# Kernel optimization log

Hardware: AMD Instinct MI355X
Metric: run time of the kernel (lower is better)

## Reference

```python
import jax, jax.numpy as jnp
import numpy as np

N, D = 2048, 64
H, W = 128, 128
NEAR, RADIUS_CLIP, BLUR = 0.01, 3.0, 0.3
A_MIN, A_MAX = 1.0 / 255.0, 0.999


def setup_inputs():
    key = jax.random.key(0)
    k = jax.random.split(key, 6)
    xy = jax.random.uniform(k[0], (N, 2), minval=-1.2, maxval=1.2)
    zz = jax.random.uniform(k[1], (N, 1), minval=3.0, maxval=5.0)
    means = jnp.concatenate([xy, zz], axis=1).astype(jnp.float32)
    quats = jax.random.normal(k[2], (N, 4), dtype=jnp.float32)
    scales = jax.random.normal(k[3], (N, 3), dtype=jnp.float32) * 0.3 - 2.2  # log-scales
    opacities = jax.random.normal(k[4], (N,), dtype=jnp.float32) * 0.5 + 1.0  # logits
    gs_features = jax.random.normal(k[5], (N, D), dtype=jnp.float32) * 0.5
    c2o = jnp.eye(4, dtype=jnp.float32)
    K = jnp.array([[200.0, 0.0, 64.0], [0.0, 200.0, 64.0], [0.0, 0.0, 1.0]], dtype=jnp.float32)
    return dict(means=means, quats=quats, scales=scales, opacities=opacities,
                gs_features=gs_features, c2o=c2o, K=K, width=W, height=H)


def _quat_to_rot(q):
    q = q / jnp.linalg.norm(q, axis=-1, keepdims=True)
    w, x, y, z = q[:, 0], q[:, 1], q[:, 2], q[:, 3]
    r0 = jnp.stack([1 - 2 * (y * y + z * z), 2 * (x * y - w * z), 2 * (x * z + w * y)], -1)
    r1 = jnp.stack([2 * (x * y + w * z), 1 - 2 * (x * x + z * z), 2 * (y * z - w * x)], -1)
    r2 = jnp.stack([2 * (x * z - w * y), 2 * (y * z + w * x), 1 - 2 * (x * x + y * y)], -1)
    return jnp.stack([r0, r1, r2], -2)  # [N,3,3]


def _rasterize(means, quats, log_scales, opac_logits, colors, viewmat, K, width, height):
    Rv, tv = viewmat[:3, :3], viewmat[:3, 3]
    fx, fy, cx, cy = K[0, 0], K[1, 1], K[0, 2], K[1, 2]
    mc = means @ Rv.T + tv                      # camera-space means [N,3]
    x, y, z = mc[:, 0], mc[:, 1], mc[:, 2]
    # 3D covariance Sigma = R S S^T R^T, rotated into camera frame
    M = _quat_to_rot(quats) * jnp.exp(log_scales)[:, None, :]
    cov_w = M @ jnp.swapaxes(M, 1, 2)           # [N,3,3]
    cov_c = jnp.einsum('ij,njk,lk->nil', Rv, cov_w, Rv)
    # perspective (EWA) Jacobian [N,2,3]
    rz = 1.0 / z
    zero = jnp.zeros_like(z)
    J = jnp.stack([jnp.stack([fx * rz, zero, -fx * x * rz * rz], -1),
                   jnp.stack([zero, fy * rz, -fy * y * rz * rz], -1)], -2)
    cov2d = jnp.einsum('nij,njk,nlk->nil', J, cov_c, J)
    a = cov2d[:, 0, 0] + BLUR
    b = cov2d[:, 0, 1]
    c = cov2d[:, 1, 1] + BLUR
    det = a * c - b * b
    cA, cB, cC = c / det, -b / det, a / det     # conic = inverse 2D covariance
    mx = fx * x * rz + cx
    my = fy * y * rz + cy
    # cull: behind near plane, degenerate, or projected 3-sigma radius below radius_clip
    lam_max = 0.5 * (a + c) + jnp.sqrt(jnp.maximum(0.25 * (a - c) ** 2 + b * b, 1e-12))
    radius = 3.0 * jnp.sqrt(lam_max)
    valid = (z > NEAR) & (det > 0) & (radius > RADIUS_CLIP)
    opac = jax.nn.sigmoid(opac_logits)
    # global front-to-back depth order (single camera)
    order = jnp.argsort(z)
    mx, my, cA, cB, cC = mx[order], my[order], cA[order], cB[order], cC[order]
    opac, valid, colors = opac[order], valid[order], colors[order]
    # per pixel-gaussian evaluation, [H,W,N]
    px = jnp.arange(width, dtype=means.dtype) + 0.5
    py = jnp.arange(height, dtype=means.dtype) + 0.5
    dx = px[None, :, None] - mx[None, None, :]
    dy = py[:, None, None] - my[None, None, :]
    sigma = 0.5 * (cA * dx * dx + cC * dy * dy) + cB * dx * dy
    alpha = jnp.minimum(opac * jnp.exp(-sigma), A_MAX)
    alpha = jnp.where((sigma >= 0) & valid & (alpha >= A_MIN), alpha, 0.0)
    # front-to-back alpha compositing: exclusive transmittance cumprod
    Tcum = jnp.cumprod(1.0 - alpha, axis=-1)
    T_excl = jnp.concatenate([jnp.ones_like(Tcum[..., :1]), Tcum[..., :-1]], axis=-1)
    out = jnp.einsum('hwn,nd->hwd', alpha * T_excl, colors)
    return out[None]  # [1,H,W,D]


def reference(means, quats, scales, opacities, gs_features, c2o, K, width, height):
    viewmat = jnp.linalg.inv(c2o)
    return _rasterize(means, quats, scales, opacities, gs_features, viewmat, K, width, height)
```

## Files before the change

### kernel.cpp

```cpp
#include <hip/hip_runtime.h>

constexpr int NG  = 2048;
constexpr int DF  = 64;
constexpr int IW  = 128;
constexpr int IH  = 128;
constexpr int SEG = 8;
constexpr int RB  = SEG * 64;
constexpr int CAP = 1024;

#define P_NEAR 0.01f
#define P_BLUR 0.3f
#define P_AMIN (1.0f/255.0f)
#define P_AMAX 0.999f

constexpr int L_T    = 0;
constexpr int L_CNT  = 512;
constexpr int L_SIDX = 528;
constexpr int L_ACC  = L_SIDX + CAP;
constexpr int L_PRM  = L_ACC;
constexpr int L_KEYS = L_PRM + CAP * 8;
constexpr int ACC_STRIDE = 66;
constexpr int L_TOTAL = L_ACC + SEG * 64 * ACC_STRIDE;

__device__ inline void invert4x4(const float* m, float* inv) {
    inv[0]  =  m[5]*m[10]*m[15] - m[5]*m[11]*m[14] - m[9]*m[6]*m[15] + m[9]*m[7]*m[14] + m[13]*m[6]*m[11] - m[13]*m[7]*m[10];
    inv[4]  = -m[4]*m[10]*m[15] + m[4]*m[11]*m[14] + m[8]*m[6]*m[15] - m[8]*m[7]*m[14] - m[12]*m[6]*m[11] + m[12]*m[7]*m[10];
    inv[8]  =  m[4]*m[9]*m[15]  - m[4]*m[11]*m[13] - m[8]*m[5]*m[15] + m[8]*m[7]*m[13] + m[12]*m[5]*m[11] - m[12]*m[7]*m[9];
    inv[12] = -m[4]*m[9]*m[14]  + m[4]*m[10]*m[13] + m[8]*m[5]*m[14] - m[8]*m[6]*m[13] - m[12]*m[5]*m[10] + m[12]*m[6]*m[9];
    inv[1]  = -m[1]*m[10]*m[15] + m[1]*m[11]*m[14] + m[9]*m[2]*m[15] - m[9]*m[3]*m[14] - m[13]*m[2]*m[11] + m[13]*m[3]*m[10];
    inv[5]  =  m[0]*m[10]*m[15] - m[0]*m[11]*m[14] - m[8]*m[2]*m[15] + m[8]*m[3]*m[14] + m[12]*m[2]*m[11] - m[12]*m[3]*m[10];
    inv[9]  = -m[0]*m[9]*m[15]  + m[0]*m[11]*m[13] + m[8]*m[1]*m[15] - m[8]*m[3]*m[13] - m[12]*m[1]*m[11] + m[12]*m[3]*m[9];
    inv[13] =  m[0]*m[9]*m[14]  - m[0]*m[10]*m[13] - m[8]*m[1]*m[14] + m[8]*m[2]*m[13] + m[12]*m[1]*m[10] - m[12]*m[2]*m[9];
    inv[2]  =  m[1]*m[6]*m[15]  - m[1]*m[7]*m[14]  - m[5]*m[2]*m[15] + m[5]*m[3]*m[14] + m[13]*m[2]*m[7]  - m[13]*m[3]*m[6];
    inv[6]  = -m[0]*m[6]*m[15]  + m[0]*m[7]*m[14]  + m[4]*m[2]*m[15] - m[4]*m[3]*m[14] - m[12]*m[2]*m[7]  + m[12]*m[3]*m[6];
    inv[10] =  m[0]*m[5]*m[15]  - m[0]*m[7]*m[13]  - m[4]*m[1]*m[15] + m[4]*m[3]*m[13] + m[12]*m[1]*m[7]  - m[12]*m[3]*m[5];
    inv[14] = -m[0]*m[5]*m[14]  + m[0]*m[6]*m[13]  + m[4]*m[1]*m[14] - m[4]*m[2]*m[13] - m[12]*m[1]*m[6]  + m[12]*m[2]*m[5];
    inv[3]  = -m[1]*m[6]*m[11]  + m[1]*m[7]*m[10]  + m[5]*m[2]*m[11] - m[5]*m[3]*m[10] - m[9]*m[2]*m[7]   + m[9]*m[3]*m[6];
    inv[7]  =  m[0]*m[6]*m[11]  - m[0]*m[7]*m[10]  - m[4]*m[2]*m[11] + m[4]*m[3]*m[10] + m[8]*m[2]*m[7]   - m[8]*m[3]*m[6];
    inv[11] = -m[0]*m[5]*m[11]  + m[0]*m[7]*m[9]   + m[4]*m[1]*m[11] - m[4]*m[3]*m[9]  - m[8]*m[1]*m[7]   + m[8]*m[3]*m[5];
    inv[15] =  m[0]*m[5]*m[10]  - m[0]*m[6]*m[9]   - m[4]*m[1]*m[10] + m[4]*m[2]*m[9]  + m[8]*m[1]*m[6]   - m[8]*m[2]*m[5];
    float det = m[0]*inv[0] + m[1]*inv[4] + m[2]*inv[8] + m[3]*inv[12];
    det = 1.0f / det;
    #pragma unroll
    for (int i = 0; i < 16; ++i) inv[i] *= det;
}

__global__ __launch_bounds__(RB) void fused_render_kernel(
    const float* __restrict__ means,  const float* __restrict__ quats,
    const float* __restrict__ scales, const float* __restrict__ opac_logits,
    const float* __restrict__ colors, const float* __restrict__ c2o,
    const float* __restrict__ Kmat,   float* __restrict__ out)
{
    extern __shared__ float lds[];
    int*                cnt  = (int*)(lds + L_CNT);
    int*                sidx = (int*)(lds + L_SIDX);
    unsigned long long* keys = (unsigned long long*)(lds + L_KEYS);
    float4*             prm4 = (float4*)(lds + L_PRM);

    const int tid  = threadIdx.x;
    const int lane = tid & 63;
    const int seg  = tid >> 6;
    const int tile = blockIdx.x;
    const int tx = (tile & 15) * 8;
    const int ty = (tile >> 4) * 8;
    const float px = tx + (lane & 7) + 0.5f;
    const float py = ty + (lane >> 3) + 0.5f;
    const float cxt = tx + 4.0f, cyt = ty + 4.0f;

    if (tid == 0) *cnt = 0;
    __syncthreads();

    {
        float inv[16];
        {
            float m[16];
            #pragma unroll
            for (int t = 0; t < 16; ++t) m[t] = c2o[t];
            invert4x4(m, inv);
        }
        const float fx = Kmat[0], fy = Kmat[4], cx = Kmat[2], cy = Kmat[5];

        for (int c = 0; c < NG / RB; ++c) {
            const int g = c * RB + tid;
            float mx = means[g*3+0], my = means[g*3+1], mz = means[g*3+2];
            float X = inv[0]*mx + inv[1]*my + inv[2]*mz  + inv[3];
            float Y = inv[4]*mx + inv[5]*my + inv[6]*mz  + inv[7];
            float Z = inv[8]*mx + inv[9]*my + inv[10]*mz + inv[11];

            float qw = quats[g*4+0], qx = quats[g*4+1], qy = quats[g*4+2], qz = quats[g*4+3];
            float qn = rsqrtf(qw*qw + qx*qx + qy*qy + qz*qz);
            qw *= qn; qx *= qn; qy *= qn; qz *= qn;
            float R00 = 1.f - 2.f*(qy*qy + qz*qz), R01 = 2.f*(qx*qy - qw*qz), R02 = 2.f*(qx*qz + qw*qy);
            float R10 = 2.f*(qx*qy + qw*qz), R11 = 1.f - 2.f*(qx*qx + qz*qz), R12 = 2.f*(qy*qz - qw*qx);
            float R20 = 2.f*(qx*qz - qw*qy), R21 = 2.f*(qy*qz + qw*qx), R22 = 1.f - 2.f*(qx*qx + qy*qy);

            float s0 = expf(scales[g*3+0]), s1 = expf(scales[g*3+1]), s2 = expf(scales[g*3+2]);
            float M00 = R00*s0, M01 = R01*s1, M02 = R02*s2;
            float M10 = R10*s0, M11 = R11*s1, M12 = R12*s2;
            float M20 = R20*s0, M21 = R21*s1, M22 = R22*s2;

            float V00 = M00*M00 + M01*M01 + M02*M02;
            float V01 = M00*M10 + M01*M11 + M02*M12;
            float V02 = M00*M20 + M01*M21 + M02*M22;
            float V11 = M10*M10 + M11*M11 + M12*M12;
            float V12 = M10*M20 + M11*M21 + M12*M22;
            float V22 = M20*M20 + M21*M21 + M22*M22;

            float Rv[3][3] = {{inv[0],inv[1],inv[2]},{inv[4],inv[5],inv[6]},{inv[8],inv[9],inv[10]}};
            float Vm[3][3] = {{V00,V01,V02},{V01,V11,V12},{V02,V12,V22}};
            float Tm[3][3], C[3][3];
            #pragma unroll
            for (int r = 0; r < 3; ++r)
                #pragma unroll
                for (int cc = 0; cc < 3; ++cc)
                    Tm[r][cc] = Rv[r][0]*Vm[0][cc] + Rv[r][1]*Vm[1][cc] + Rv[r][2]*Vm[2][cc];
            #pragma unroll
            for (int r = 0; r < 3; ++r)
                #pragma unroll
                for (int cc = 0; cc < 3; ++cc)
                    C[r][cc] = Tm[r][0]*Rv[cc][0] + Tm[r][1]*Rv[cc][1] + Tm[r][2]*Rv[cc][2];

            float rz = 1.0f / Z;
            float j00 = fx*rz, j02 = -fx*X*rz*rz;
            float j11 = fy*rz, j12 = -fy*Y*rz*rz;

            float c00 = j00*j00*C[0][0] + 2.f*j00*j02*C[0][2] + j02*j02*C[2][2];
            float c01 = j00*j11*C[0][1] + j00*j12*C[0][2] + j02*j11*C[1][2] + j02*j12*C[2][2];
            float c11 = j11*j11*C[1][1] + 2.f*j11*j12*C[1][2] + j12*j12*C[2][2];

            float a = c00 + P_BLUR;
            float b = c01;
            float cc_ = c11 + P_BLUR;
            float det = a*cc_ - b*b;

            float pmx = fx*X*rz + cx;
            float pmy = fy*Y*rz + cy;

            float lam = 0.5f*(a + cc_) + sqrtf(fmaxf(0.25f*(a - cc_)*(a - cc_) + b*b, 1e-12f));
            float radius = 3.0f * sqrtf(lam);
            bool valid = (Z > P_NEAR) && (det > 0.0f) && (radius > 3.0f);

            float op = 1.0f / (1.0f + expf(-opac_logits[g]));

            bool sel = false;
            float cA = 0.f, cB = 0.f, cC2 = 0.f;
            if (valid) {
                float rdet = 1.0f / det;
                cA = cc_ * rdet; cB = -b * rdet; cC2 = a * rdet;
                float smax = logf(255.0f * op);
                if (smax > 0.f) {
                    float rx = sqrtf(2.f * a   * smax) * 1.0001f + 1e-3f;
                    float ry = sqrtf(2.f * cc_ * smax) * 1.0001f + 1e-3f;
                    sel = (fabsf(pmx - cxt) <= rx + 3.5f) && (fabsf(pmy - cyt) <= ry + 3.5f);
                }
            }

            unsigned long long m = __ballot(sel);
            int wbase = 0;
            if (lane == 0 && m) wbase = atomicAdd(cnt, (int)__popcll(m));
            wbase = __shfl(wbase, 0);
            if (sel) {
                int pos = wbase + (int)__popcll(m & ((1ull << lane) - 1ull));
                if (pos < CAP) {
                    prm4[pos*2]   = make_float4(pmx, pmy, cA, cB);
                    prm4[pos*2+1] = make_float4(cC2, op, __int_as_float(g), 0.f);
                    keys[pos] = ((unsigned long long)__float_as_uint(Z) << 32) | (unsigned)g;
                }
            }
        }
    }
    __syncthreads();
    int L = *cnt;
    if (L > CAP) L = CAP;

    {
        int padL = (L + 1) & ~1;
        if (tid < padL - L) keys[L + tid] = ~0ull;
        __syncthreads();
        const ulonglong2* k2 = (const ulonglong2*)keys;
        for (int k = tid; k < L; k += RB) {
            unsigned long long kk = keys[k];
            int rank = 0;
            #pragma unroll 2
            for (int c = 0; c < padL / 2; ++c) {
                ulonglong2 q = k2[c];
                rank += (q.x < kk) + (q.y < kk);
            }
            sidx[rank] = k;
        }
    }
    __syncthreads();

    float acc[64];
    #pragma unroll
    for (int f = 0; f < 64; ++f) acc[f] = 0.f;
    float T = 1.0f;

    {
        const int r0 = (seg * L) >> 3;
        const int r1 = ((seg + 1) * L) >> 3;
        const float4* cp4 = (const float4*)colors;
        if (r1 > r0) {
            int k = sidx[r0];
            float4 e0 = prm4[k*2], e1 = prm4[k*2+1];
            for (int r = r0; r < r1; ++r) {
                int kn = (r + 1 < r1) ? sidx[r + 1] : k;
                float4 f0 = prm4[kn*2], f1 = prm4[kn*2+1];

                const float4* crow = cp4 + (size_t)(unsigned)__float_as_int(e1.z) * 16;
                float4 cbuf[16];
                #pragma unroll
                for (int q = 0; q < 16; ++q) cbuf[q] = crow[q];

                float dx = px - e0.x, dy = py - e0.y;
                float sig = 0.5f*(e0.z*dx*dx + e1.x*dy*dy) + e0.w*dx*dy;
                float al = fminf(e1.y * __expf(-sig), P_AMAX);
                al = (sig >= 0.f && al >= P_AMIN) ? al : 0.f;

                if (__ballot(al > 0.f)) {
                    float wv = T * al;
                    #pragma unroll
                    for (int q = 0; q < 16; ++q) {
                        acc[4*q+0] = fmaf(wv, cbuf[q].x, acc[4*q+0]);
                        acc[4*q+1] = fmaf(wv, cbuf[q].y, acc[4*q+1]);
                        acc[4*q+2] = fmaf(wv, cbuf[q].z, acc[4*q+2]);
                        acc[4*q+3] = fmaf(wv, cbuf[q].w, acc[4*q+3]);
                    }
                    T *= (1.f - al);
                    if (!__ballot(T >= 1e-6f)) break;
                }
                e0 = f0; e1 = f1; k = kn;
            }
        }
    }

    __syncthreads();
    {
        float* ab = lds + L_ACC + (size_t)(seg * 64 + lane) * ACC_STRIDE;
        #pragma unroll
        for (int q = 0; q < 32; ++q)
            *(float2*)(ab + 2*q) = make_float2(acc[2*q], acc[2*q+1]);
        lds[L_T + seg*64 + lane] = T;
    }
    __syncthreads();

    {
        int p  = tid >> 3;
        int f0 = (tid & 7) * 8;
        float r[8];
        const float* ab = lds + L_ACC + (size_t)((SEG-1)*64 + p) * ACC_STRIDE + f0;
        #pragma unroll
        for (int j = 0; j < 4; ++j) {
            float2 u = *(const float2*)(ab + 2*j);
            r[2*j] = u.x; r[2*j+1] = u.y;
        }
        #pragma unroll
        for (int s = SEG - 2; s >= 0; --s) {
            float Ts = lds[L_T + s*64 + p];
            const float* as_ = lds + L_ACC + (size_t)(s*64 + p) * ACC_STRIDE + f0;
            #pragma unroll
            for (int j = 0; j < 4; ++j) {
                float2 u = *(const float2*)(as_ + 2*j);
                r[2*j]   = fmaf(Ts, r[2*j],   u.x);
                r[2*j+1] = fmaf(Ts, r[2*j+1], u.y);
            }
        }
        int pyg = ty + (p >> 3), pxg = tx + (p & 7);
        float* op_ = out + (size_t)(pyg * IW + pxg) * DF + f0;
        *(float4*)op_       = make_float4(r[0], r[1], r[2], r[3]);
        *(float4*)(op_ + 4) = make_float4(r[4], r[5], r[6], r[7]);
    }
}

extern "C" void kernel_launch(void* const* d_in, const int* in_sizes, int n_in,
                              void* d_out, int out_size, void* d_ws, size_t ws_size,
                              hipStream_t stream) {
    const float* means  = (const float*)d_in[0];
    const float* quats  = (const float*)d_in[1];
    const float* scales = (const float*)d_in[2];
    const float* opac   = (const float*)d_in[3];
    const float* colors = (const float*)d_in[4];
    const float* c2o    = (const float*)d_in[5];
    const float* Kmat   = (const float*)d_in[6];
    float* out = (float*)d_out;
    (void)d_ws; (void)ws_size;

    (void)hipFuncSetAttribute((const void*)fused_render_kernel,
                              hipFuncAttributeMaxDynamicSharedMemorySize,
                              L_TOTAL * 4);

    fused_render_kernel<<<IH*IW/64, RB, L_TOTAL*4, stream>>>(
        means, quats, scales, opac, colors, c2o, Kmat, out);
}
```

Measured before the change: 118.7 us.

## Split each tile's depth range across 16 waves with a chunked LDS reduction

Each 8x8 tile's sorted Gaussian list is now split into 16 depth segments instead of 8, so the block runs 1024 threads and each wave composites a shorter run of Gaussians. The per-segment accumulator merge is redone in four 16-feature chunks with a narrower LDS stride, so the reduction buffer stays small while sharing space with the parameter area. The sort loop drops to a single pass per thread, since the block now has at least as many threads as list entries. The aim is more latency hiding per CU on the serial compositing loop. In exchange it risks register spills, because the 64-float accumulator must fit a 1024-thread block, and it adds extra barriers and wasted work in later segments that cannot stop early on transmittance.

```diff
diff --git a/kernel.cpp b/kernel.cpp
--- a/kernel.cpp
+++ b/kernel.cpp
@@ -4,7 +4,7 @@
 constexpr int DF  = 64;
 constexpr int IW  = 128;
 constexpr int IH  = 128;
-constexpr int SEG = 8;
+constexpr int SEG = 16;
 constexpr int RB  = SEG * 64;
 constexpr int CAP = 1024;
 
@@ -14,13 +14,14 @@
 #define P_AMAX 0.999f
 
 constexpr int L_T    = 0;
-constexpr int L_CNT  = 512;
-constexpr int L_SIDX = 528;
-constexpr int L_ACC  = L_SIDX + CAP;
-constexpr int L_PRM  = L_ACC;
+constexpr int L_CNT  = 1024;
+constexpr int L_SIDX = 1040;
+constexpr int L_OVL  = L_SIDX + CAP;
+constexpr int L_PRM  = L_OVL;
 constexpr int L_KEYS = L_PRM + CAP * 8;
-constexpr int ACC_STRIDE = 66;
-constexpr int L_TOTAL = L_ACC + SEG * 64 * ACC_STRIDE;
+constexpr int L_ACC  = L_OVL;
+constexpr int ACC_ST = 18;
+constexpr int L_TOTAL = L_OVL + SEG * 64 * ACC_ST;
 
 __device__ inline void invert4x4(const float* m, float* inv) {
     inv[0]  =  m[5]*m[10]*m[15] - m[5]*m[11]*m[14] - m[9]*m[6]*m[15] + m[9]*m[7]*m[14] + m[13]*m[6]*m[11] - m[13]*m[7]*m[10];
@@ -80,6 +81,7 @@
         }
         const float fx = Kmat[0], fy = Kmat[4], cx = Kmat[2], cy = Kmat[5];
 
+        #pragma unroll
         for (int c = 0; c < NG / RB; ++c) {
             const int g = c * RB + tid;
             float mx = means[g*3+0], my = means[g*3+1], mz = means[g*3+2];
@@ -178,15 +180,15 @@
         if (tid < padL - L) keys[L + tid] = ~0ull;
         __syncthreads();
         const ulonglong2* k2 = (const ulonglong2*)keys;
-        for (int k = tid; k < L; k += RB) {
-            unsigned long long kk = keys[k];
+        if (tid < L) {
+            unsigned long long kk = keys[tid];
             int rank = 0;
             #pragma unroll 2
             for (int c = 0; c < padL / 2; ++c) {
                 ulonglong2 q = k2[c];
                 rank += (q.x < kk) + (q.y < kk);
             }
-            sidx[rank] = k;
+            sidx[rank] = tid;
         }
     }
     __syncthreads();
@@ -197,8 +199,8 @@
     float T = 1.0f;
 
     {
-        const int r0 = (seg * L) >> 3;
-        const int r1 = ((seg + 1) * L) >> 3;
+        const int r0 = (seg * L) >> 4;
+        const int r1 = ((seg + 1) * L) >> 4;
         const float4* cp4 = (const float4*)colors;
         if (r1 > r0) {
             int k = sidx[r0];
@@ -234,41 +236,32 @@
         }
     }
 
-    __syncthreads();
-    {
-        float* ab = lds + L_ACC + (size_t)(seg * 64 + lane) * ACC_STRIDE;
+    lds[L_T + seg*64 + lane] = T;
+    __syncthreads();
+
+    const int p_  = tid >> 4;
+    const int f_  = tid & 15;
+    const int pyg = ty + (p_ >> 3), pxg = tx + (p_ & 7);
+    float* opix = out + (size_t)(pyg * IW + pxg) * DF + f_;
+
+    #pragma unroll
+    for (int c = 0; c < 4; ++c) {
+        float* ab = lds + L_ACC + (size_t)(seg * 64 + lane) * ACC_ST;
         #pragma unroll
-        for (int q = 0; q < 32; ++q)
-            *(float2*)(ab + 2*q) = make_float2(acc[2*q], acc[2*q+1]);
-        lds[L_T + seg*64 + lane] = T;
-    }
-    __syncthreads();
-
-    {
-        int p  = tid >> 3;
-        int f0 = (tid & 7) * 8;
-        float r[8];
-        const float* ab = lds + L_ACC + (size_t)((SEG-1)*64 + p) * ACC_STRIDE + f0;
-        #pragma unroll
-        for (int j = 0; j < 4; ++j) {
-            float2 u = *(const float2*)(ab + 2*j);
-            r[2*j] = u.x; r[2*j+1] = u.y;
-        }
-        #pragma unroll
-        for (int s = SEG - 2; s >= 0; --s) {
-            float Ts = lds[L_T + s*64 + p];
-            const float* as_ = lds + L_ACC + (size_t)(s*64 + p) * ACC_STRIDE + f0;
-            #pragma unroll
-            for (int j = 0; j < 4; ++j) {
-                float2 u = *(const float2*)(as_ + 2*j);
-                r[2*j]   = fmaf(Ts, r[2*j],   u.x);
-                r[2*j+1] = fmaf(Ts, r[2*j+1], u.y);
-            }
-        }
-        int pyg = ty + (p >> 3), pxg = tx + (p & 7);
-        float* op_ = out + (size_t)(pyg * IW + pxg) * DF + f0;
-        *(float4*)op_       = make_float4(r[0], r[1], r[2], r[3]);
-        *(float4*)(op_ + 4) = make_float4(r[4], r[5], r[6], r[7]);
+        for (int q = 0; q < 8; ++q)
+            *(float2*)(ab + 2*q) = make_float2(acc[16*c + 2*q], acc[16*c + 2*q + 1]);
+        __syncthreads();
+
+        {
+            float r = lds[L_ACC + (size_t)(15*64 + p_) * ACC_ST + f_];
+            #pragma unroll
+            for (int s = SEG - 2; s >= 0; --s) {
+                float Ts = lds[L_T + s*64 + p_];
+                r = fmaf(Ts, r, lds[L_ACC + (size_t)(s*64 + p_) * ACC_ST + f_]);
+            }
+            opix[c*16] = r;
+        }
+        if (c < 3) __syncthreads();
     }
 }
 
```

Result: slower. 229.7 us (+93.5%).
